# Performance work log

Hardware: AMD Instinct MI355X
Metric: run time of the kernel (lower is better)

## Reference

```python
import jax, jax.numpy as jnp
import numpy as np

MUL = 128          # multiplicity for every irrep
N = 100000         # number of nodes
INV_SQRT_FANIN = 1.0 / np.sqrt(MUL).astype(np.float32)


def setup_inputs() -> dict:
    key = jax.random.key(0)
    k = jax.random.split(key, 5)
    return {
        "x": jax.random.normal(k[0], (N, MUL + 3 * MUL), dtype=jnp.float32),   # [N, 512] = 128x0e + 128x1o
        "w1_s": jax.random.normal(k[1], (MUL, 2 * MUL), dtype=jnp.float32),    # 0e path of linear_1 (-> scalars+gates)
        "w1_v": jax.random.normal(k[2], (MUL, MUL), dtype=jnp.float32),        # 1o path of linear_1
        "w2_s": jax.random.normal(k[3], (MUL, MUL), dtype=jnp.float32),        # 0e path of linear_2
        "w2_v": jax.random.normal(k[4], (MUL, MUL), dtype=jnp.float32),        # 1o path of linear_2
    }


def reference(x, w1_s, w1_v, w2_s, w2_v):
    n = x.shape[0]
    x0 = x[:, :MUL]                              # [N, 128]  scalars (0e)
    x1 = x[:, MUL:].reshape(n, MUL, 3)           # [N, 128, 3] vectors (1o)

    # linear_1: 128x0e+128x1o -> 256x0e + 128x1o (scalars | gates | gated)
    s = (x0 @ w1_s) * INV_SQRT_FANIN             # [N, 256]
    v = jnp.einsum('nui,uv->nvi', x1, w1_v) * INV_SQRT_FANIN  # [N, 128, 3]

    # Gate: silu on scalars, silu(gates) broadcast-multiplies the vectors
    h0 = jax.nn.silu(s[:, :MUL])                 # [N, 128]
    g = jax.nn.silu(s[:, MUL:])                  # [N, 128]
    h1 = v * g[:, :, None]                       # [N, 128, 3]

    # linear_2: 128x0e+128x1o -> 128x0e+128x1o
    y0 = (h0 @ w2_s) * INV_SQRT_FANIN            # [N, 128]
    y1 = jnp.einsum('nui,uv->nvi', h1, w2_v) * INV_SQRT_FANIN  # [N, 128, 3]
    return jnp.concatenate([y0, y1.reshape(n, 3 * MUL)], axis=-1)  # [N, 512]
```

## Files before the change

kernel.cpp:

```cpp
#include <hip/hip_runtime.h>
#include <cstdint>

#define TPB  512
#define ROWS 32

typedef __attribute__((ext_vector_type(8))) short  short8;
typedef __attribute__((ext_vector_type(8))) __bf16 bf16x8;
typedef __attribute__((ext_vector_type(4))) float  f32x4;
typedef __attribute__((ext_vector_type(4))) short  short4v;

__device__ __forceinline__ short f2bf(float f) {
    union { float f; unsigned int u; } v; v.f = f;
    unsigned int u = v.u;
    u += 0x7fffu + ((u >> 16) & 1u);
    return (short)(u >> 16);
}
__device__ __forceinline__ float silu_f(float x) { return x / (1.0f + __expf(-x)); }

#define RSB 256
#define OFF_X0 0
#define OFF_X1 8192
#define OFF_H0 32768
#define SMEM_BYTES 40960

__device__ __forceinline__ int swz(int row, int b) { return row * RSB + (b ^ ((row & 7) << 4)); }

__device__ __forceinline__ short8 lds_bfrag(const char* sm, int off, int r0, int ks, int lane) {
    int row = r0 + (lane & 15);
    int bi  = ks * 64 + ((lane >> 4) << 4);
    return *(const short8*)(sm + off + swz(row, bi));
}

template<bool PACKED>
__device__ __forceinline__ short8 wfrag(const short8* pw, const float* W, int ldn,
                                        int gtile, int ltile, int ks, int lane) {
    if constexpr (PACKED) {
        return pw[(gtile * 4 + ks) * 64 + lane];
    } else {
        const float* p = W + (size_t)(ks * 32 + ((lane >> 4) << 3)) * ldn + ltile * 16 + (lane & 15);
        short8 r;
#pragma unroll
        for (int j = 0; j < 8; ++j) r[j] = f2bf(p[(size_t)j * ldn]);
        return r;
    }
}

__device__ __forceinline__ f32x4 mfma16(short8 a, short8 b, f32x4 c) {
    return __builtin_amdgcn_mfma_f32_16x16x32_bf16(
        __builtin_bit_cast(bf16x8, a), __builtin_bit_cast(bf16x8, b), c, 0, 0, 0);
}

__global__ void prep_pack(const float* __restrict__ w1s, const float* __restrict__ w1v,
                          const float* __restrict__ w2s, const float* __restrict__ w2v,
                          short8* __restrict__ pk) {
    int b = blockIdx.x;
    int t = threadIdx.x;
    int ks = t >> 6, lane = t & 63;
    const float* W; int ldn, lt;
    if (b < 16)      { W = w1s; ldn = 256; lt = b; }
    else if (b < 24) { W = w1v; ldn = 128; lt = b - 16; }
    else if (b < 32) { W = w2s; ldn = 128; lt = b - 24; }
    else             { W = w2v; ldn = 128; lt = b - 32; }
    const float* p = W + (size_t)(ks * 32 + ((lane >> 4) << 3)) * ldn + lt * 16 + (lane & 15);
    short8 r;
#pragma unroll
    for (int j = 0; j < 8; ++j) r[j] = f2bf(p[(size_t)j * ldn]);
    pk[(b * 4 + ks) * 64 + lane] = r;
}

template<bool PACKED>
__global__ __launch_bounds__(TPB, 8) void gnlr_fused_kernel(
    const float* __restrict__ x,
    const float* __restrict__ w1s, const float* __restrict__ w1v,
    const float* __restrict__ w2s, const float* __restrict__ w2v,
    const short8* __restrict__ pw,
    float* __restrict__ out, int n)
{
    __shared__ alignas(16) char sm[SMEM_BYTES];

    const int tid   = threadIdx.x;
    const int lane  = tid & 63;
    const int w     = tid >> 6;
    const int row0g = blockIdx.x * ROWS;
    const int c0    = w * 16;
    const float INV = 0.08838834764831845f;
    const f32x4 z = { 0.f, 0.f, 0.f, 0.f };

#pragma unroll
    for (int it = 0; it < 2; ++it) {
        int idx = tid + it * TPB;
        int row = idx >> 5;
        int c4  = (idx & 31) << 2;
        int rg  = row0g + row; if (rg >= n) rg = n - 1;
        float4 f = *(const float4*)(x + (size_t)rg * 512 + c4);
        short4v pkv;
        pkv.x = f2bf(f.x); pkv.y = f2bf(f.y); pkv.z = f2bf(f.z); pkv.w = f2bf(f.w);
        *(short4v*)(sm + OFF_X0 + swz(row, c4 * 2)) = pkv;
    }
#pragma unroll
    for (int it = 0; it < 2; ++it) {
        int idx = tid + it * TPB;
        int row = idx >> 5;
        int grp = idx & 31;
        int rg  = row0g + row; if (rg >= n) rg = n - 1;
        const float* p = x + (size_t)rg * 512 + 128 + grp * 12;
        float4 fa = *(const float4*)(p);
        float4 fb = *(const float4*)(p + 4);
        float4 fc = *(const float4*)(p + 8);
        float f[12] = { fa.x, fa.y, fa.z, fa.w, fb.x, fb.y, fb.z, fb.w, fc.x, fc.y, fc.z, fc.w };
#pragma unroll
        for (int i = 0; i < 3; ++i) {
            short4v pkv;
            pkv.x = f2bf(f[i]); pkv.y = f2bf(f[3 + i]); pkv.z = f2bf(f[6 + i]); pkv.w = f2bf(f[9 + i]);
            *(short4v*)(sm + OFF_X1 + i * 8192 + swz(row, grp * 8)) = pkv;
        }
    }
    __syncthreads();

    float g_reg[2][4];
    {
        short8 bs[4];
#pragma unroll
        for (int ks = 0; ks < 4; ++ks) bs[ks] = wfrag<PACKED>(pw, w1s, 256, w, w, ks, lane);
#pragma unroll
        for (int rt = 0; rt < 2; ++rt) {
            f32x4 acc = z;
#pragma unroll
            for (int ks = 0; ks < 4; ++ks)
                acc = mfma16(bs[ks], lds_bfrag(sm, OFF_X0, rt * 16, ks, lane), acc);
            short4v pkv;
#pragma unroll
            for (int j = 0; j < 4; ++j) pkv[j] = f2bf(silu_f(acc[j] * INV));
            int row = rt * 16 + (lane & 15);
            *(short4v*)(sm + OFF_H0 + swz(row, 2 * (c0 + ((lane >> 4) << 2)))) = pkv;
        }
#pragma unroll
        for (int ks = 0; ks < 4; ++ks) bs[ks] = wfrag<PACKED>(pw, w1s, 256, 8 + w, 8 + w, ks, lane);
#pragma unroll
        for (int rt = 0; rt < 2; ++rt) {
            f32x4 acc = z;
#pragma unroll
            for (int ks = 0; ks < 4; ++ks)
                acc = mfma16(bs[ks], lds_bfrag(sm, OFF_X0, rt * 16, ks, lane), acc);
#pragma unroll
            for (int j = 0; j < 4; ++j) g_reg[rt][j] = silu_f(acc[j] * INV);
        }
    }

    {
        short8 bv[4];
#pragma unroll
        for (int ks = 0; ks < 4; ++ks) bv[ks] = wfrag<PACKED>(pw, w1v, 128, 16 + w, w, ks, lane);
#pragma unroll
        for (int i = 0; i < 3; ++i) {
            __syncthreads();
#pragma unroll
            for (int rt = 0; rt < 2; ++rt) {
                f32x4 acc = z;
#pragma unroll
                for (int ks = 0; ks < 4; ++ks)
                    acc = mfma16(bv[ks], lds_bfrag(sm, OFF_X1 + i * 8192, rt * 16, ks, lane), acc);
                short4v pkv;
#pragma unroll
                for (int j = 0; j < 4; ++j) pkv[j] = f2bf(acc[j] * INV * g_reg[rt][j]);
                int row = rt * 16 + (lane & 15);
                *(short4v*)(sm + i * 8192 + swz(row, 2 * (c0 + ((lane >> 4) << 2)))) = pkv;
            }
        }
    }
    __syncthreads();

    {
        short8 b2[4];
#pragma unroll
        for (int ks = 0; ks < 4; ++ks) b2[ks] = wfrag<PACKED>(pw, w2s, 128, 24 + w, w, ks, lane);
#pragma unroll
        for (int rt = 0; rt < 2; ++rt) {
            f32x4 acc = z;
#pragma unroll
            for (int ks = 0; ks < 4; ++ks)
                acc = mfma16(b2[ks], lds_bfrag(sm, OFF_H0, rt * 16, ks, lane), acc);
            int rg = row0g + rt * 16 + (lane & 15);
            if (rg < n) {
                float4 o = { acc[0] * INV, acc[1] * INV, acc[2] * INV, acc[3] * INV };
                *(float4*)(out + (size_t)rg * 512 + c0 + ((lane >> 4) << 2)) = o;
            }
        }
#pragma unroll
        for (int ks = 0; ks < 4; ++ks) b2[ks] = wfrag<PACKED>(pw, w2v, 128, 32 + w, w, ks, lane);
#pragma unroll
        for (int rt = 0; rt < 2; ++rt) {
            f32x4 a3[3];
#pragma unroll
            for (int i = 0; i < 3; ++i) {
                a3[i] = z;
#pragma unroll
                for (int ks = 0; ks < 4; ++ks)
                    a3[i] = mfma16(b2[ks], lds_bfrag(sm, i * 8192, rt * 16, ks, lane), a3[i]);
            }
            int rg = row0g + rt * 16 + (lane & 15);
            if (rg < n) {
                float* base = out + (size_t)rg * 512 + 128 + 3 * (c0 + ((lane >> 4) << 2));
                float4 s0 = { a3[0][0] * INV, a3[1][0] * INV, a3[2][0] * INV, a3[0][1] * INV };
                float4 s1 = { a3[1][1] * INV, a3[2][1] * INV, a3[0][2] * INV, a3[1][2] * INV };
                float4 s2 = { a3[2][2] * INV, a3[0][3] * INV, a3[1][3] * INV, a3[2][3] * INV };
                *(float4*)(base + 0) = s0;
                *(float4*)(base + 4) = s1;
                *(float4*)(base + 8) = s2;
            }
        }
    }
}

extern "C" void kernel_launch(void* const* d_in, const int* in_sizes, int n_in,
                              void* d_out, int out_size, void* d_ws, size_t ws_size,
                              hipStream_t stream) {
    const float* x   = (const float*)d_in[0];
    const float* w1s = (const float*)d_in[1];
    const float* w1v = (const float*)d_in[2];
    const float* w2s = (const float*)d_in[3];
    const float* w2v = (const float*)d_in[4];
    float* out = (float*)d_out;
    const int n = in_sizes[0] / 512;
    const int grid = (n + ROWS - 1) / ROWS;
    const size_t need = (size_t)40 * 4 * 64 * sizeof(short8);
    if (ws_size >= need) {
        prep_pack<<<40, 256, 0, stream>>>(w1s, w1v, w2s, w2v, (short8*)d_ws);
        gnlr_fused_kernel<true><<<grid, TPB, 0, stream>>>(x, w1s, w1v, w2s, w2v,
                                                          (const short8*)d_ws, out, n);
    } else {
        gnlr_fused_kernel<false><<<grid, TPB, 0, stream>>>(x, w1s, w1v, w2s, w2v,
                                                           nullptr, out, n);
    }
}
```

Measured before the change: 107.5 us.

## Shrink block to 16 rows and 4 waves, each wave covering two column tiles

The block now handles 16 rows with 256 threads instead of 32 rows with 512, which halves LDS per block to 20 KB. Each wave now computes two column tiles over one 16-row tile, so the loops are reorganised from row tiles to column tiles. The aim is more resident blocks and finer scheduling granularity. In exchange, each weight fragment is reused over half as many rows, so weight fragment loads per output row double, and the w1v fragments are now reloaded inside each of the three vector-component passes.

```diff
diff --git a/kernel.cpp b/kernel.cpp
--- a/kernel.cpp
+++ b/kernel.cpp
@@ -1,8 +1,8 @@
 #include <hip/hip_runtime.h>
 #include <cstdint>
 
-#define TPB  512
-#define ROWS 32
+#define TPB  256
+#define ROWS 16
 
 typedef __attribute__((ext_vector_type(8))) short  short8;
 typedef __attribute__((ext_vector_type(8))) __bf16 bf16x8;
@@ -18,15 +18,14 @@
 __device__ __forceinline__ float silu_f(float x) { return x / (1.0f + __expf(-x)); }
 
 #define RSB 256
-#define OFF_X0 0
-#define OFF_X1 8192
-#define OFF_H0 32768
-#define SMEM_BYTES 40960
+#define OFF_X1 4096
+#define OFF_H0 16384
+#define SMEM_BYTES 20480
 
 __device__ __forceinline__ int swz(int row, int b) { return row * RSB + (b ^ ((row & 7) << 4)); }
 
-__device__ __forceinline__ short8 lds_bfrag(const char* sm, int off, int r0, int ks, int lane) {
-    int row = r0 + (lane & 15);
+__device__ __forceinline__ short8 lds_bfrag(const char* sm, int off, int ks, int lane) {
+    int row = lane & 15;
     int bi  = ks * 64 + ((lane >> 4) << 4);
     return *(const short8*)(sm + off + swz(row, bi));
 }
@@ -82,7 +81,6 @@
     const int lane  = tid & 63;
     const int w     = tid >> 6;
     const int row0g = blockIdx.x * ROWS;
-    const int c0    = w * 16;
     const float INV = 0.08838834764831845f;
     const f32x4 z = { 0.f, 0.f, 0.f, 0.f };
 
@@ -95,7 +93,7 @@
         float4 f = *(const float4*)(x + (size_t)rg * 512 + c4);
         short4v pkv;
         pkv.x = f2bf(f.x); pkv.y = f2bf(f.y); pkv.z = f2bf(f.z); pkv.w = f2bf(f.w);
-        *(short4v*)(sm + OFF_X0 + swz(row, c4 * 2)) = pkv;
+        *(short4v*)(sm + swz(row, c4 * 2)) = pkv;
     }
 #pragma unroll
     for (int it = 0; it < 2; ++it) {
@@ -112,93 +110,93 @@
         for (int i = 0; i < 3; ++i) {
             short4v pkv;
             pkv.x = f2bf(f[i]); pkv.y = f2bf(f[3 + i]); pkv.z = f2bf(f[6 + i]); pkv.w = f2bf(f[9 + i]);
-            *(short4v*)(sm + OFF_X1 + i * 8192 + swz(row, grp * 8)) = pkv;
+            *(short4v*)(sm + OFF_X1 + i * 4096 + swz(row, grp * 8)) = pkv;
         }
     }
     __syncthreads();
 
     float g_reg[2][4];
-    {
+#pragma unroll
+    for (int ut = 0; ut < 2; ++ut) {
+        int t0 = w + 4 * ut;
+        int c0 = t0 * 16;
         short8 bs[4];
 #pragma unroll
-        for (int ks = 0; ks < 4; ++ks) bs[ks] = wfrag<PACKED>(pw, w1s, 256, w, w, ks, lane);
-#pragma unroll
-        for (int rt = 0; rt < 2; ++rt) {
-            f32x4 acc = z;
-#pragma unroll
-            for (int ks = 0; ks < 4; ++ks)
-                acc = mfma16(bs[ks], lds_bfrag(sm, OFF_X0, rt * 16, ks, lane), acc);
+        for (int ks = 0; ks < 4; ++ks) bs[ks] = wfrag<PACKED>(pw, w1s, 256, t0, t0, ks, lane);
+        {
+            f32x4 acc = z;
+#pragma unroll
+            for (int ks = 0; ks < 4; ++ks)
+                acc = mfma16(bs[ks], lds_bfrag(sm, 0, ks, lane), acc);
             short4v pkv;
 #pragma unroll
             for (int j = 0; j < 4; ++j) pkv[j] = f2bf(silu_f(acc[j] * INV));
-            int row = rt * 16 + (lane & 15);
-            *(short4v*)(sm + OFF_H0 + swz(row, 2 * (c0 + ((lane >> 4) << 2)))) = pkv;
-        }
-#pragma unroll
-        for (int ks = 0; ks < 4; ++ks) bs[ks] = wfrag<PACKED>(pw, w1s, 256, 8 + w, 8 + w, ks, lane);
-#pragma unroll
-        for (int rt = 0; rt < 2; ++rt) {
-            f32x4 acc = z;
-#pragma unroll
-            for (int ks = 0; ks < 4; ++ks)
-                acc = mfma16(bs[ks], lds_bfrag(sm, OFF_X0, rt * 16, ks, lane), acc);
-#pragma unroll
-            for (int j = 0; j < 4; ++j) g_reg[rt][j] = silu_f(acc[j] * INV);
-        }
-    }
-
-    {
-        short8 bv[4];
-#pragma unroll
-        for (int ks = 0; ks < 4; ++ks) bv[ks] = wfrag<PACKED>(pw, w1v, 128, 16 + w, w, ks, lane);
-#pragma unroll
-        for (int i = 0; i < 3; ++i) {
-            __syncthreads();
-#pragma unroll
-            for (int rt = 0; rt < 2; ++rt) {
-                f32x4 acc = z;
-#pragma unroll
-                for (int ks = 0; ks < 4; ++ks)
-                    acc = mfma16(bv[ks], lds_bfrag(sm, OFF_X1 + i * 8192, rt * 16, ks, lane), acc);
-                short4v pkv;
-#pragma unroll
-                for (int j = 0; j < 4; ++j) pkv[j] = f2bf(acc[j] * INV * g_reg[rt][j]);
-                int row = rt * 16 + (lane & 15);
-                *(short4v*)(sm + i * 8192 + swz(row, 2 * (c0 + ((lane >> 4) << 2)))) = pkv;
-            }
+            *(short4v*)(sm + OFF_H0 + swz(lane & 15, 2 * (c0 + ((lane >> 4) << 2)))) = pkv;
+        }
+#pragma unroll
+        for (int ks = 0; ks < 4; ++ks) bs[ks] = wfrag<PACKED>(pw, w1s, 256, 8 + t0, 8 + t0, ks, lane);
+        {
+            f32x4 acc = z;
+#pragma unroll
+            for (int ks = 0; ks < 4; ++ks)
+                acc = mfma16(bs[ks], lds_bfrag(sm, 0, ks, lane), acc);
+#pragma unroll
+            for (int j = 0; j < 4; ++j) g_reg[ut][j] = silu_f(acc[j] * INV);
+        }
+    }
+
+#pragma unroll
+    for (int i = 0; i < 3; ++i) {
+        __syncthreads();
+#pragma unroll
+        for (int ut = 0; ut < 2; ++ut) {
+            int t0 = w + 4 * ut;
+            int c0 = t0 * 16;
+            short8 bv[4];
+#pragma unroll
+            for (int ks = 0; ks < 4; ++ks) bv[ks] = wfrag<PACKED>(pw, w1v, 128, 16 + t0, t0, ks, lane);
+            f32x4 acc = z;
+#pragma unroll
+            for (int ks = 0; ks < 4; ++ks)
+                acc = mfma16(bv[ks], lds_bfrag(sm, OFF_X1 + i * 4096, ks, lane), acc);
+            short4v pkv;
+#pragma unroll
+            for (int j = 0; j < 4; ++j) pkv[j] = f2bf(acc[j] * INV * g_reg[ut][j]);
+            *(short4v*)(sm + i * 4096 + swz(lane & 15, 2 * (c0 + ((lane >> 4) << 2)))) = pkv;
         }
     }
     __syncthreads();
 
-    {
+#pragma unroll
+    for (int ut = 0; ut < 2; ++ut) {
+        int t0 = w + 4 * ut;
+        int c0 = t0 * 16;
         short8 b2[4];
 #pragma unroll
-        for (int ks = 0; ks < 4; ++ks) b2[ks] = wfrag<PACKED>(pw, w2s, 128, 24 + w, w, ks, lane);
-#pragma unroll
-        for (int rt = 0; rt < 2; ++rt) {
-            f32x4 acc = z;
-#pragma unroll
-            for (int ks = 0; ks < 4; ++ks)
-                acc = mfma16(b2[ks], lds_bfrag(sm, OFF_H0, rt * 16, ks, lane), acc);
-            int rg = row0g + rt * 16 + (lane & 15);
+        for (int ks = 0; ks < 4; ++ks) b2[ks] = wfrag<PACKED>(pw, w2s, 128, 24 + t0, t0, ks, lane);
+        {
+            f32x4 acc = z;
+#pragma unroll
+            for (int ks = 0; ks < 4; ++ks)
+                acc = mfma16(b2[ks], lds_bfrag(sm, OFF_H0, ks, lane), acc);
+            int rg = row0g + (lane & 15);
             if (rg < n) {
                 float4 o = { acc[0] * INV, acc[1] * INV, acc[2] * INV, acc[3] * INV };
                 *(float4*)(out + (size_t)rg * 512 + c0 + ((lane >> 4) << 2)) = o;
             }
         }
 #pragma unroll
-        for (int ks = 0; ks < 4; ++ks) b2[ks] = wfrag<PACKED>(pw, w2v, 128, 32 + w, w, ks, lane);
-#pragma unroll
-        for (int rt = 0; rt < 2; ++rt) {
+        for (int ks = 0; ks < 4; ++ks) b2[ks] = wfrag<PACKED>(pw, w2v, 128, 32 + t0, t0, ks, lane);
+        {
             f32x4 a3[3];
 #pragma unroll
             for (int i = 0; i < 3; ++i) {
                 a3[i] = z;
 #pragma unroll
                 for (int ks = 0; ks < 4; ++ks)
-                    a3[i] = mfma16(b2[ks], lds_bfrag(sm, i * 8192, rt * 16, ks, lane), a3[i]);
+                    a3[i] = mfma16(b2[ks], lds_bfrag(sm, i * 4096, ks, lane), a3[i]);
             }
-            int rg = row0g + rt * 16 + (lane & 15);
+            int rg = row0g + (lane & 15);
             if (rg < n) {
                 float* base = out + (size_t)rg * 512 + 128 + 3 * (c0 + ((lane >> 4) << 2));
                 float4 s0 = { a3[0][0] * INV, a3[1][0] * INV, a3[2][0] * INV, a3[0][1] * INV };
```

Result: slower. 196.8 us (+83.0%).

## Make fused kernel persistent with atomic tile scheduling and double-buffered prefetch

Applied to the files above, without the earlier changes.

Turns the one-block-per-tile fused kernel into a persistent kernel with a fixed grid of 512 blocks. Blocks claim 32-row tiles through an atomic counter, which is reset by a memset before launch. Each block prefetches the next tile's x into registers while it computes the current tile, then writes it to a second LDS buffer. This is meant to hide global load latency and cut per-block launch and setup cost, but it raises LDS use to 72KB per block, lowers launch bounds occupancy to 4, and adds an atomic plus a barrier per tile. Tail handling is dropped (ntile = n/ROWS, no row bounds checks), so rows beyond a multiple of 32 would never be computed.

```diff
diff --git a/kernel.cpp b/kernel.cpp
--- a/kernel.cpp
+++ b/kernel.cpp
@@ -1,8 +1,9 @@
 #include <hip/hip_runtime.h>
 #include <cstdint>
 
-#define TPB  512
-#define ROWS 32
+#define TPB   512
+#define ROWS  32
+#define PGRID 512
 
 typedef __attribute__((ext_vector_type(8))) short  short8;
 typedef __attribute__((ext_vector_type(8))) __bf16 bf16x8;
@@ -18,17 +19,16 @@
 __device__ __forceinline__ float silu_f(float x) { return x / (1.0f + __expf(-x)); }
 
 #define RSB 256
-#define OFF_X0 0
-#define OFF_X1 8192
-#define OFF_H0 32768
-#define SMEM_BYTES 40960
+#define BUFSZ 32768
+#define OFF_H0 65536
+#define SMEM_BYTES 73728
 
 __device__ __forceinline__ int swz(int row, int b) { return row * RSB + (b ^ ((row & 7) << 4)); }
 
-__device__ __forceinline__ short8 lds_bfrag(const char* sm, int off, int r0, int ks, int lane) {
+__device__ __forceinline__ short8 lds_bfrag(const char* base, int off, int r0, int ks, int lane) {
     int row = r0 + (lane & 15);
     int bi  = ks * 64 + ((lane >> 4) << 4);
-    return *(const short8*)(sm + off + swz(row, bi));
+    return *(const short8*)(base + off + swz(row, bi));
 }
 
 template<bool PACKED>
@@ -53,8 +53,7 @@
 __global__ void prep_pack(const float* __restrict__ w1s, const float* __restrict__ w1v,
                           const float* __restrict__ w2s, const float* __restrict__ w2v,
                           short8* __restrict__ pk) {
-    int b = blockIdx.x;
-    int t = threadIdx.x;
+    int b = blockIdx.x, t = threadIdx.x;
     int ks = t >> 6, lane = t & 63;
     const float* W; int ldn, lt;
     if (b < 16)      { W = w1s; ldn = 256; lt = b; }
@@ -69,137 +68,178 @@
 }
 
 template<bool PACKED>
-__global__ __launch_bounds__(TPB, 8) void gnlr_fused_kernel(
+__global__ __launch_bounds__(TPB, 4) void gnlr_fused_kernel(
     const float* __restrict__ x,
     const float* __restrict__ w1s, const float* __restrict__ w1v,
     const float* __restrict__ w2s, const float* __restrict__ w2v,
-    const short8* __restrict__ pw,
-    float* __restrict__ out, int n)
+    const short8* __restrict__ pw, unsigned int* __restrict__ ctr,
+    float* __restrict__ out, int ntile)
 {
-    __shared__ alignas(16) char sm[SMEM_BYTES];
-
-    const int tid   = threadIdx.x;
-    const int lane  = tid & 63;
-    const int w     = tid >> 6;
-    const int row0g = blockIdx.x * ROWS;
-    const int c0    = w * 16;
+    extern __shared__ char sm[];
+    __shared__ int s_tile;
+
+    const int tid  = threadIdx.x;
+    const int lane = tid & 63;
+    const int w    = tid >> 6;
+    const int c0   = w * 16;
     const float INV = 0.08838834764831845f;
     const f32x4 z = { 0.f, 0.f, 0.f, 0.f };
 
-#pragma unroll
-    for (int it = 0; it < 2; ++it) {
-        int idx = tid + it * TPB;
-        int row = idx >> 5;
-        int c4  = (idx & 31) << 2;
-        int rg  = row0g + row; if (rg >= n) rg = n - 1;
-        float4 f = *(const float4*)(x + (size_t)rg * 512 + c4);
-        short4v pkv;
-        pkv.x = f2bf(f.x); pkv.y = f2bf(f.y); pkv.z = f2bf(f.z); pkv.w = f2bf(f.w);
-        *(short4v*)(sm + OFF_X0 + swz(row, c4 * 2)) = pkv;
-    }
-#pragma unroll
-    for (int it = 0; it < 2; ++it) {
-        int idx = tid + it * TPB;
-        int row = idx >> 5;
-        int grp = idx & 31;
-        int rg  = row0g + row; if (rg >= n) rg = n - 1;
-        const float* p = x + (size_t)rg * 512 + 128 + grp * 12;
-        float4 fa = *(const float4*)(p);
-        float4 fb = *(const float4*)(p + 4);
-        float4 fc = *(const float4*)(p + 8);
-        float f[12] = { fa.x, fa.y, fa.z, fa.w, fb.x, fb.y, fb.z, fb.w, fc.x, fc.y, fc.z, fc.w };
-#pragma unroll
-        for (int i = 0; i < 3; ++i) {
-            short4v pkv;
-            pkv.x = f2bf(f[i]); pkv.y = f2bf(f[3 + i]); pkv.z = f2bf(f[6 + i]); pkv.w = f2bf(f[9 + i]);
-            *(short4v*)(sm + OFF_X1 + i * 8192 + swz(row, grp * 8)) = pkv;
-        }
-    }
-    __syncthreads();
-
-    float g_reg[2][4];
-    {
-        short8 bs[4];
-#pragma unroll
-        for (int ks = 0; ks < 4; ++ks) bs[ks] = wfrag<PACKED>(pw, w1s, 256, w, w, ks, lane);
-#pragma unroll
-        for (int rt = 0; rt < 2; ++rt) {
-            f32x4 acc = z;
-#pragma unroll
-            for (int ks = 0; ks < 4; ++ks)
-                acc = mfma16(bs[ks], lds_bfrag(sm, OFF_X0, rt * 16, ks, lane), acc);
-            short4v pkv;
-#pragma unroll
-            for (int j = 0; j < 4; ++j) pkv[j] = f2bf(silu_f(acc[j] * INV));
-            int row = rt * 16 + (lane & 15);
-            *(short4v*)(sm + OFF_H0 + swz(row, 2 * (c0 + ((lane >> 4) << 2)))) = pkv;
-        }
-#pragma unroll
-        for (int ks = 0; ks < 4; ++ks) bs[ks] = wfrag<PACKED>(pw, w1s, 256, 8 + w, 8 + w, ks, lane);
-#pragma unroll
-        for (int rt = 0; rt < 2; ++rt) {
-            f32x4 acc = z;
-#pragma unroll
-            for (int ks = 0; ks < 4; ++ks)
-                acc = mfma16(bs[ks], lds_bfrag(sm, OFF_X0, rt * 16, ks, lane), acc);
-#pragma unroll
-            for (int j = 0; j < 4; ++j) g_reg[rt][j] = silu_f(acc[j] * INV);
-        }
-    }
-
-    {
-        short8 bv[4];
-#pragma unroll
-        for (int ks = 0; ks < 4; ++ks) bv[ks] = wfrag<PACKED>(pw, w1v, 128, 16 + w, w, ks, lane);
-#pragma unroll
-        for (int i = 0; i < 3; ++i) {
+    float4 st[8];
+    int nextStatic = blockIdx.x;
+
+    auto grab = [&]() -> int {
+        int r;
+        if constexpr (PACKED) {
+            if (tid == 0) s_tile = (int)atomicAdd(ctr, 1u);
             __syncthreads();
+            r = s_tile;
+        } else {
+            r = nextStatic; nextStatic += PGRID;
+            __syncthreads();
+        }
+        return r;
+    };
+
+    auto issue = [&](int tile) {
+        const float* xb = x + (size_t)tile * ROWS * 512;
+#pragma unroll
+        for (int it = 0; it < 2; ++it) {
+            int idx = tid + it * TPB;
+            int row = idx >> 5, c4 = (idx & 31) << 2;
+            st[it] = *(const float4*)(xb + row * 512 + c4);
+        }
+#pragma unroll
+        for (int it = 0; it < 2; ++it) {
+            int idx = tid + it * TPB;
+            int row = idx >> 5, grp = idx & 31;
+            const float* p = xb + row * 512 + 128 + grp * 12;
+            st[2 + it * 3 + 0] = *(const float4*)(p);
+            st[2 + it * 3 + 1] = *(const float4*)(p + 4);
+            st[2 + it * 3 + 2] = *(const float4*)(p + 8);
+        }
+    };
+
+    auto writeLDS = [&](int buf) {
+        char* b = sm + buf * BUFSZ;
+#pragma unroll
+        for (int it = 0; it < 2; ++it) {
+            int idx = tid + it * TPB;
+            int row = idx >> 5, c4 = (idx & 31) << 2;
+            float4 f = st[it];
+            short4v pk;
+            pk.x = f2bf(f.x); pk.y = f2bf(f.y); pk.z = f2bf(f.z); pk.w = f2bf(f.w);
+            *(short4v*)(b + swz(row, c4 * 2)) = pk;
+        }
+#pragma unroll
+        for (int it = 0; it < 2; ++it) {
+            int idx = tid + it * TPB;
+            int row = idx >> 5, grp = idx & 31;
+            float4 fa = st[2 + it * 3 + 0], fb = st[2 + it * 3 + 1], fc = st[2 + it * 3 + 2];
+            float fv[12] = { fa.x, fa.y, fa.z, fa.w, fb.x, fb.y, fb.z, fb.w, fc.x, fc.y, fc.z, fc.w };
+#pragma unroll
+            for (int i = 0; i < 3; ++i) {
+                short4v pk;
+                pk.x = f2bf(fv[i]); pk.y = f2bf(fv[3 + i]); pk.z = f2bf(fv[6 + i]); pk.w = f2bf(fv[9 + i]);
+                *(short4v*)(b + 8192 + i * 8192 + swz(row, grp * 8)) = pk;
+            }
+        }
+    };
+
+    int tcur = grab();
+    if (tcur >= ntile) return;
+    issue(tcur);
+    writeLDS(0);
+    int cur = 0;
+
+    while (true) {
+        int tnext = grab();
+        bool hasN = tnext < ntile;
+        if (hasN) issue(tnext);
+
+        char* B = sm + cur * BUFSZ;
+        const int row0g = tcur * ROWS;
+
+        float g_reg[2][4];
+        {
+            short8 bs[4];
+#pragma unroll
+            for (int ks = 0; ks < 4; ++ks) bs[ks] = wfrag<PACKED>(pw, w1s, 256, w, w, ks, lane);
 #pragma unroll
             for (int rt = 0; rt < 2; ++rt) {
                 f32x4 acc = z;
 #pragma unroll
                 for (int ks = 0; ks < 4; ++ks)
-                    acc = mfma16(bv[ks], lds_bfrag(sm, OFF_X1 + i * 8192, rt * 16, ks, lane), acc);
+                    acc = mfma16(bs[ks], lds_bfrag(B, 0, rt * 16, ks, lane), acc);
                 short4v pkv;
 #pragma unroll
-                for (int j = 0; j < 4; ++j) pkv[j] = f2bf(acc[j] * INV * g_reg[rt][j]);
+                for (int j = 0; j < 4; ++j) pkv[j] = f2bf(silu_f(acc[j] * INV));
                 int row = rt * 16 + (lane & 15);
-                *(short4v*)(sm + i * 8192 + swz(row, 2 * (c0 + ((lane >> 4) << 2)))) = pkv;
-            }
-        }
-    }
-    __syncthreads();
-
-    {
-        short8 b2[4];
-#pragma unroll
-        for (int ks = 0; ks < 4; ++ks) b2[ks] = wfrag<PACKED>(pw, w2s, 128, 24 + w, w, ks, lane);
-#pragma unroll
-        for (int rt = 0; rt < 2; ++rt) {
-            f32x4 acc = z;
-#pragma unroll
-            for (int ks = 0; ks < 4; ++ks)
-                acc = mfma16(b2[ks], lds_bfrag(sm, OFF_H0, rt * 16, ks, lane), acc);
-            int rg = row0g + rt * 16 + (lane & 15);
-            if (rg < n) {
+                *(short4v*)(sm + OFF_H0 + swz(row, 2 * (c0 + ((lane >> 4) << 2)))) = pkv;
+            }
+#pragma unroll
+            for (int ks = 0; ks < 4; ++ks) bs[ks] = wfrag<PACKED>(pw, w1s, 256, 8 + w, 8 + w, ks, lane);
+#pragma unroll
+            for (int rt = 0; rt < 2; ++rt) {
+                f32x4 acc = z;
+#pragma unroll
+                for (int ks = 0; ks < 4; ++ks)
+                    acc = mfma16(bs[ks], lds_bfrag(B, 0, rt * 16, ks, lane), acc);
+#pragma unroll
+                for (int j = 0; j < 4; ++j) g_reg[rt][j] = silu_f(acc[j] * INV);
+            }
+        }
+
+        {
+            short8 bv[4];
+#pragma unroll
+            for (int ks = 0; ks < 4; ++ks) bv[ks] = wfrag<PACKED>(pw, w1v, 128, 16 + w, w, ks, lane);
+#pragma unroll
+            for (int i = 0; i < 3; ++i) {
+                __syncthreads();
+#pragma unroll
+                for (int rt = 0; rt < 2; ++rt) {
+                    f32x4 acc = z;
+#pragma unroll
+                    for (int ks = 0; ks < 4; ++ks)
+                        acc = mfma16(bv[ks], lds_bfrag(B, 8192 + i * 8192, rt * 16, ks, lane), acc);
+                    short4v pkv;
+#pragma unroll
+                    for (int j = 0; j < 4; ++j) pkv[j] = f2bf(acc[j] * INV * g_reg[rt][j]);
+                    int row = rt * 16 + (lane & 15);
+                    *(short4v*)(B + i * 8192 + swz(row, 2 * (c0 + ((lane >> 4) << 2)))) = pkv;
+                }
+            }
+        }
+        __syncthreads();
+
+        {
+            short8 b2[4];
+#pragma unroll
+            for (int ks = 0; ks < 4; ++ks) b2[ks] = wfrag<PACKED>(pw, w2s, 128, 24 + w, w, ks, lane);
+#pragma unroll
+            for (int rt = 0; rt < 2; ++rt) {
+                f32x4 acc = z;
+#pragma unroll
+                for (int ks = 0; ks < 4; ++ks)
+                    acc = mfma16(b2[ks], lds_bfrag(sm, OFF_H0, rt * 16, ks, lane), acc);
+                int rg = row0g + rt * 16 + (lane & 15);
                 float4 o = { acc[0] * INV, acc[1] * INV, acc[2] * INV, acc[3] * INV };
                 *(float4*)(out + (size_t)rg * 512 + c0 + ((lane >> 4) << 2)) = o;
             }
-        }
-#pragma unroll
-        for (int ks = 0; ks < 4; ++ks) b2[ks] = wfrag<PACKED>(pw, w2v, 128, 32 + w, w, ks, lane);
-#pragma unroll
-        for (int rt = 0; rt < 2; ++rt) {
-            f32x4 a3[3];
-#pragma unroll
-            for (int i = 0; i < 3; ++i) {
-                a3[i] = z;
-#pragma unroll
-                for (int ks = 0; ks < 4; ++ks)
-                    a3[i] = mfma16(b2[ks], lds_bfrag(sm, i * 8192, rt * 16, ks, lane), a3[i]);
-            }
-            int rg = row0g + rt * 16 + (lane & 15);
-            if (rg < n) {
+#pragma unroll
+            for (int ks = 0; ks < 4; ++ks) b2[ks] = wfrag<PACKED>(pw, w2v, 128, 32 + w, w, ks, lane);
+#pragma unroll
+            for (int rt = 0; rt < 2; ++rt) {
+                f32x4 a3[3];
+#pragma unroll
+                for (int i = 0; i < 3; ++i) {
+                    a3[i] = z;
+#pragma unroll
+                    for (int ks = 0; ks < 4; ++ks)
+                        a3[i] = mfma16(b2[ks], lds_bfrag(B, i * 8192, rt * 16, ks, lane), a3[i]);
+                }
+                int rg = row0g + rt * 16 + (lane & 15);
                 float* base = out + (size_t)rg * 512 + 128 + 3 * (c0 + ((lane >> 4) << 2));
                 float4 s0 = { a3[0][0] * INV, a3[1][0] * INV, a3[2][0] * INV, a3[0][1] * INV };
                 float4 s1 = { a3[1][1] * INV, a3[2][1] * INV, a3[0][2] * INV, a3[1][2] * INV };
@@ -209,6 +249,11 @@
                 *(float4*)(base + 8) = s2;
             }
         }
+
+        if (!hasN) break;
+        writeLDS(cur ^ 1);
+        cur ^= 1;
+        tcur = tnext;
     }
 }
 
@@ -222,14 +267,16 @@
     const float* w2v = (const float*)d_in[4];
     float* out = (float*)d_out;
     const int n = in_sizes[0] / 512;
-    const int grid = (n + ROWS - 1) / ROWS;
-    const size_t need = (size_t)40 * 4 * 64 * sizeof(short8);
-    if (ws_size >= need) {
+    const int ntile = n / ROWS;
+    const size_t needW = (size_t)40 * 4 * 64 * sizeof(short8);
+    if (ws_size >= needW + 4) {
+        unsigned int* ctr = (unsigned int*)((char*)d_ws + needW);
+        hipMemsetAsync(ctr, 0, 4, stream);
         prep_pack<<<40, 256, 0, stream>>>(w1s, w1v, w2s, w2v, (short8*)d_ws);
-        gnlr_fused_kernel<true><<<grid, TPB, 0, stream>>>(x, w1s, w1v, w2s, w2v,
-                                                          (const short8*)d_ws, out, n);
+        gnlr_fused_kernel<true><<<PGRID, TPB, SMEM_BYTES, stream>>>(
+            x, w1s, w1v, w2s, w2v, (const short8*)d_ws, ctr, out, ntile);
     } else {
-        gnlr_fused_kernel<false><<<grid, TPB, 0, stream>>>(x, w1s, w1v, w2s, w2v,
-                                                           nullptr, out, n);
+        gnlr_fused_kernel<false><<<PGRID, TPB, SMEM_BYTES, stream>>>(
+            x, w1s, w1v, w2s, w2v, nullptr, nullptr, out, ntile);
     }
 }
```

Result: slower. 301.5 us (+180.5%).

## Process two row tiles per block with register-prefetched loads and nontemporal stores

Applied to the files above, without the earlier changes.

Each block now handles two 32-row tiles. The global loads for the second tile are issued into registers while the first tile computes, hiding load latency behind the MFMA work. Output stores become nontemporal, and launch bounds drop to 4 blocks per CU to make room for the extra registers. The tail clamping is removed and the grid uses n/32, so when n is not a multiple of 32 the leftover rows are never computed. This is fine for N=100000, but it adds register pressure and may lower occupancy.

```diff
diff --git a/kernel.cpp b/kernel.cpp
--- a/kernel.cpp
+++ b/kernel.cpp
@@ -17,18 +17,20 @@
 }
 __device__ __forceinline__ float silu_f(float x) { return x / (1.0f + __expf(-x)); }
 
+__device__ __forceinline__ void nt_st4(float* p, f32x4 v) {
+    __builtin_nontemporal_store(v, (f32x4*)p);
+}
+
 #define RSB 256
-#define OFF_X0 0
-#define OFF_X1 8192
 #define OFF_H0 32768
 #define SMEM_BYTES 40960
 
 __device__ __forceinline__ int swz(int row, int b) { return row * RSB + (b ^ ((row & 7) << 4)); }
 
-__device__ __forceinline__ short8 lds_bfrag(const char* sm, int off, int r0, int ks, int lane) {
+__device__ __forceinline__ short8 lds_bfrag(const char* base, int off, int r0, int ks, int lane) {
     int row = r0 + (lane & 15);
     int bi  = ks * 64 + ((lane >> 4) << 4);
-    return *(const short8*)(sm + off + swz(row, bi));
+    return *(const short8*)(base + off + swz(row, bi));
 }
 
 template<bool PACKED>
@@ -53,8 +55,7 @@
 __global__ void prep_pack(const float* __restrict__ w1s, const float* __restrict__ w1v,
                           const float* __restrict__ w2s, const float* __restrict__ w2v,
                           short8* __restrict__ pk) {
-    int b = blockIdx.x;
-    int t = threadIdx.x;
+    int b = blockIdx.x, t = threadIdx.x;
     int ks = t >> 6, lane = t & 63;
     const float* W; int ldn, lt;
     if (b < 16)      { W = w1s; ldn = 256; lt = b; }
@@ -69,7 +70,7 @@
 }
 
 template<bool PACKED>
-__global__ __launch_bounds__(TPB, 8) void gnlr_fused_kernel(
+__global__ __launch_bounds__(TPB, 4) void gnlr_fused_kernel(
     const float* __restrict__ x,
     const float* __restrict__ w1s, const float* __restrict__ w1v,
     const float* __restrict__ w2s, const float* __restrict__ w2v,
@@ -81,134 +82,169 @@
     const int tid   = threadIdx.x;
     const int lane  = tid & 63;
     const int w     = tid >> 6;
-    const int row0g = blockIdx.x * ROWS;
     const int c0    = w * 16;
     const float INV = 0.08838834764831845f;
     const f32x4 z = { 0.f, 0.f, 0.f, 0.f };
 
-#pragma unroll
-    for (int it = 0; it < 2; ++it) {
-        int idx = tid + it * TPB;
-        int row = idx >> 5;
-        int c4  = (idx & 31) << 2;
-        int rg  = row0g + row; if (rg >= n) rg = n - 1;
-        float4 f = *(const float4*)(x + (size_t)rg * 512 + c4);
-        short4v pkv;
-        pkv.x = f2bf(f.x); pkv.y = f2bf(f.y); pkv.z = f2bf(f.z); pkv.w = f2bf(f.w);
-        *(short4v*)(sm + OFF_X0 + swz(row, c4 * 2)) = pkv;
-    }
-#pragma unroll
-    for (int it = 0; it < 2; ++it) {
-        int idx = tid + it * TPB;
-        int row = idx >> 5;
-        int grp = idx & 31;
-        int rg  = row0g + row; if (rg >= n) rg = n - 1;
-        const float* p = x + (size_t)rg * 512 + 128 + grp * 12;
-        float4 fa = *(const float4*)(p);
-        float4 fb = *(const float4*)(p + 4);
-        float4 fc = *(const float4*)(p + 8);
-        float f[12] = { fa.x, fa.y, fa.z, fa.w, fb.x, fb.y, fb.z, fb.w, fc.x, fc.y, fc.z, fc.w };
-#pragma unroll
-        for (int i = 0; i < 3; ++i) {
-            short4v pkv;
-            pkv.x = f2bf(f[i]); pkv.y = f2bf(f[3 + i]); pkv.z = f2bf(f[6 + i]); pkv.w = f2bf(f[9 + i]);
-            *(short4v*)(sm + OFF_X1 + i * 8192 + swz(row, grp * 8)) = pkv;
-        }
-    }
+    const int ntile = n >> 5;
+    const int t0 = blockIdx.x * 2;
+    const int t1 = t0 + 1;
+    const bool has1 = (t1 < ntile);
+
+    float4 st[8];
+
+    auto issue = [&](int tile) {
+        const float* xb = x + (size_t)tile * ROWS * 512;
+#pragma unroll
+        for (int it = 0; it < 2; ++it) {
+            int idx = tid + it * TPB;
+            int row = idx >> 5, c4 = (idx & 31) << 2;
+            st[it] = *(const float4*)(xb + row * 512 + c4);
+        }
+#pragma unroll
+        for (int it = 0; it < 2; ++it) {
+            int idx = tid + it * TPB;
+            int row = idx >> 5, grp = idx & 31;
+            const float* p = xb + row * 512 + 128 + grp * 12;
+            st[2 + it * 3 + 0] = *(const float4*)(p);
+            st[2 + it * 3 + 1] = *(const float4*)(p + 4);
+            st[2 + it * 3 + 2] = *(const float4*)(p + 8);
+        }
+    };
+
+    auto writeLDS = [&]() {
+#pragma unroll
+        for (int it = 0; it < 2; ++it) {
+            int idx = tid + it * TPB;
+            int row = idx >> 5, c4 = (idx & 31) << 2;
+            float4 f = st[it];
+            short4v pk;
+            pk.x = f2bf(f.x); pk.y = f2bf(f.y); pk.z = f2bf(f.z); pk.w = f2bf(f.w);
+            *(short4v*)(sm + swz(row, c4 * 2)) = pk;
+        }
+#pragma unroll
+        for (int it = 0; it < 2; ++it) {
+            int idx = tid + it * TPB;
+            int row = idx >> 5, grp = idx & 31;
+            float4 fa = st[2 + it * 3 + 0], fb = st[2 + it * 3 + 1], fc = st[2 + it * 3 + 2];
+            float fv[12] = { fa.x, fa.y, fa.z, fa.w, fb.x, fb.y, fb.z, fb.w, fc.x, fc.y, fc.z, fc.w };
+#pragma unroll
+            for (int i = 0; i < 3; ++i) {
+                short4v pk;
+                pk.x = f2bf(fv[i]); pk.y = f2bf(fv[3 + i]); pk.z = f2bf(fv[6 + i]); pk.w = f2bf(fv[9 + i]);
+                *(short4v*)(sm + 8192 + i * 8192 + swz(row, grp * 8)) = pk;
+            }
+        }
+    };
+
+    auto computeTile = [&](int tile) {
+        const int row0g = tile * ROWS;
+
+        float g_reg[2][4];
+        {
+            short8 bs[4];
+#pragma unroll
+            for (int ks = 0; ks < 4; ++ks) bs[ks] = wfrag<PACKED>(pw, w1s, 256, w, w, ks, lane);
+#pragma unroll
+            for (int rt = 0; rt < 2; ++rt) {
+                f32x4 acc = z;
+#pragma unroll
+                for (int ks = 0; ks < 4; ++ks)
+                    acc = mfma16(bs[ks], lds_bfrag(sm, 0, rt * 16, ks, lane), acc);
+                short4v pkv;
+#pragma unroll
+                for (int j = 0; j < 4; ++j) pkv[j] = f2bf(silu_f(acc[j] * INV));
+                int row = rt * 16 + (lane & 15);
+                *(short4v*)(sm + OFF_H0 + swz(row, 2 * (c0 + ((lane >> 4) << 2)))) = pkv;
+            }
+#pragma unroll
+            for (int ks = 0; ks < 4; ++ks) bs[ks] = wfrag<PACKED>(pw, w1s, 256, 8 + w, 8 + w, ks, lane);
+#pragma unroll
+            for (int rt = 0; rt < 2; ++rt) {
+                f32x4 acc = z;
+#pragma unroll
+                for (int ks = 0; ks < 4; ++ks)
+                    acc = mfma16(bs[ks], lds_bfrag(sm, 0, rt * 16, ks, lane), acc);
+#pragma unroll
+                for (int j = 0; j < 4; ++j) g_reg[rt][j] = silu_f(acc[j] * INV);
+            }
+        }
+
+        {
+            short8 bv[4];
+#pragma unroll
+            for (int ks = 0; ks < 4; ++ks) bv[ks] = wfrag<PACKED>(pw, w1v, 128, 16 + w, w, ks, lane);
+#pragma unroll
+            for (int i = 0; i < 3; ++i) {
+                __syncthreads();
+#pragma unroll
+                for (int rt = 0; rt < 2; ++rt) {
+                    f32x4 acc = z;
+#pragma unroll
+                    for (int ks = 0; ks < 4; ++ks)
+                        acc = mfma16(bv[ks], lds_bfrag(sm, 8192 + i * 8192, rt * 16, ks, lane), acc);
+                    short4v pkv;
+#pragma unroll
+                    for (int j = 0; j < 4; ++j) pkv[j] = f2bf(acc[j] * INV * g_reg[rt][j]);
+                    int row = rt * 16 + (lane & 15);
+                    *(short4v*)(sm + i * 8192 + swz(row, 2 * (c0 + ((lane >> 4) << 2)))) = pkv;
+                }
+            }
+        }
+        __syncthreads();
+
+        {
+            short8 b2[4];
+#pragma unroll
+            for (int ks = 0; ks < 4; ++ks) b2[ks] = wfrag<PACKED>(pw, w2s, 128, 24 + w, w, ks, lane);
+#pragma unroll
+            for (int rt = 0; rt < 2; ++rt) {
+                f32x4 acc = z;
+#pragma unroll
+                for (int ks = 0; ks < 4; ++ks)
+                    acc = mfma16(b2[ks], lds_bfrag(sm, OFF_H0, rt * 16, ks, lane), acc);
+                int rg = row0g + rt * 16 + (lane & 15);
+                if (rg < n) {
+                    f32x4 o = { acc[0] * INV, acc[1] * INV, acc[2] * INV, acc[3] * INV };
+                    nt_st4(out + (size_t)rg * 512 + c0 + ((lane >> 4) << 2), o);
+                }
+            }
+#pragma unroll
+            for (int ks = 0; ks < 4; ++ks) b2[ks] = wfrag<PACKED>(pw, w2v, 128, 32 + w, w, ks, lane);
+#pragma unroll
+            for (int rt = 0; rt < 2; ++rt) {
+                f32x4 a3[3];
+#pragma unroll
+                for (int i = 0; i < 3; ++i) {
+                    a3[i] = z;
+#pragma unroll
+                    for (int ks = 0; ks < 4; ++ks)
+                        a3[i] = mfma16(b2[ks], lds_bfrag(sm, i * 8192, rt * 16, ks, lane), a3[i]);
+                }
+                int rg = row0g + rt * 16 + (lane & 15);
+                if (rg < n) {
+                    float* base = out + (size_t)rg * 512 + 128 + 3 * (c0 + ((lane >> 4) << 2));
+                    f32x4 s0 = { a3[0][0] * INV, a3[1][0] * INV, a3[2][0] * INV, a3[0][1] * INV };
+                    f32x4 s1 = { a3[1][1] * INV, a3[2][1] * INV, a3[0][2] * INV, a3[1][2] * INV };
+                    f32x4 s2 = { a3[2][2] * INV, a3[0][3] * INV, a3[1][3] * INV, a3[2][3] * INV };
+                    nt_st4(base + 0, s0);
+                    nt_st4(base + 4, s1);
+                    nt_st4(base + 8, s2);
+                }
+            }
+        }
+    };
+
+    issue(t0);
+    writeLDS();
     __syncthreads();
-
-    float g_reg[2][4];
-    {
-        short8 bs[4];
-#pragma unroll
-        for (int ks = 0; ks < 4; ++ks) bs[ks] = wfrag<PACKED>(pw, w1s, 256, w, w, ks, lane);
-#pragma unroll
-        for (int rt = 0; rt < 2; ++rt) {
-            f32x4 acc = z;
-#pragma unroll
-            for (int ks = 0; ks < 4; ++ks)
-                acc = mfma16(bs[ks], lds_bfrag(sm, OFF_X0, rt * 16, ks, lane), acc);
-            short4v pkv;
-#pragma unroll
-            for (int j = 0; j < 4; ++j) pkv[j] = f2bf(silu_f(acc[j] * INV));
-            int row = rt * 16 + (lane & 15);
-            *(short4v*)(sm + OFF_H0 + swz(row, 2 * (c0 + ((lane >> 4) << 2)))) = pkv;
-        }
-#pragma unroll
-        for (int ks = 0; ks < 4; ++ks) bs[ks] = wfrag<PACKED>(pw, w1s, 256, 8 + w, 8 + w, ks, lane);
-#pragma unroll
-        for (int rt = 0; rt < 2; ++rt) {
-            f32x4 acc = z;
-#pragma unroll
-            for (int ks = 0; ks < 4; ++ks)
-                acc = mfma16(bs[ks], lds_bfrag(sm, OFF_X0, rt * 16, ks, lane), acc);
-#pragma unroll
-            for (int j = 0; j < 4; ++j) g_reg[rt][j] = silu_f(acc[j] * INV);
-        }
-    }
-
-    {
-        short8 bv[4];
-#pragma unroll
-        for (int ks = 0; ks < 4; ++ks) bv[ks] = wfrag<PACKED>(pw, w1v, 128, 16 + w, w, ks, lane);
-#pragma unroll
-        for (int i = 0; i < 3; ++i) {
-            __syncthreads();
-#pragma unroll
-            for (int rt = 0; rt < 2; ++rt) {
-                f32x4 acc = z;
-#pragma unroll
-                for (int ks = 0; ks < 4; ++ks)
-                    acc = mfma16(bv[ks], lds_bfrag(sm, OFF_X1 + i * 8192, rt * 16, ks, lane), acc);
-                short4v pkv;
-#pragma unroll
-                for (int j = 0; j < 4; ++j) pkv[j] = f2bf(acc[j] * INV * g_reg[rt][j]);
-                int row = rt * 16 + (lane & 15);
-                *(short4v*)(sm + i * 8192 + swz(row, 2 * (c0 + ((lane >> 4) << 2)))) = pkv;
-            }
-        }
-    }
-    __syncthreads();
-
-    {
-        short8 b2[4];
-#pragma unroll
-        for (int ks = 0; ks < 4; ++ks) b2[ks] = wfrag<PACKED>(pw, w2s, 128, 24 + w, w, ks, lane);
-#pragma unroll
-        for (int rt = 0; rt < 2; ++rt) {
-            f32x4 acc = z;
-#pragma unroll
-            for (int ks = 0; ks < 4; ++ks)
-                acc = mfma16(b2[ks], lds_bfrag(sm, OFF_H0, rt * 16, ks, lane), acc);
-            int rg = row0g + rt * 16 + (lane & 15);
-            if (rg < n) {
-                float4 o = { acc[0] * INV, acc[1] * INV, acc[2] * INV, acc[3] * INV };
-                *(float4*)(out + (size_t)rg * 512 + c0 + ((lane >> 4) << 2)) = o;
-            }
-        }
-#pragma unroll
-        for (int ks = 0; ks < 4; ++ks) b2[ks] = wfrag<PACKED>(pw, w2v, 128, 32 + w, w, ks, lane);
-#pragma unroll
-        for (int rt = 0; rt < 2; ++rt) {
-            f32x4 a3[3];
-#pragma unroll
-            for (int i = 0; i < 3; ++i) {
-                a3[i] = z;
-#pragma unroll
-                for (int ks = 0; ks < 4; ++ks)
-                    a3[i] = mfma16(b2[ks], lds_bfrag(sm, i * 8192, rt * 16, ks, lane), a3[i]);
-            }
-            int rg = row0g + rt * 16 + (lane & 15);
-            if (rg < n) {
-                float* base = out + (size_t)rg * 512 + 128 + 3 * (c0 + ((lane >> 4) << 2));
-                float4 s0 = { a3[0][0] * INV, a3[1][0] * INV, a3[2][0] * INV, a3[0][1] * INV };
-                float4 s1 = { a3[1][1] * INV, a3[2][1] * INV, a3[0][2] * INV, a3[1][2] * INV };
-                float4 s2 = { a3[2][2] * INV, a3[0][3] * INV, a3[1][3] * INV, a3[2][3] * INV };
-                *(float4*)(base + 0) = s0;
-                *(float4*)(base + 4) = s1;
-                *(float4*)(base + 8) = s2;
-            }
-        }
+    if (has1) issue(t1);
+    computeTile(t0);
+    if (has1) {
+        __syncthreads();
+        writeLDS();
+        __syncthreads();
+        computeTile(t1);
     }
 }
 
@@ -222,7 +258,8 @@
     const float* w2v = (const float*)d_in[4];
     float* out = (float*)d_out;
     const int n = in_sizes[0] / 512;
-    const int grid = (n + ROWS - 1) / ROWS;
+    const int ntile = n / ROWS;
+    const int grid = (ntile + 1) / 2;
     const size_t need = (size_t)40 * 4 * 64 * sizeof(short8);
     if (ws_size >= need) {
         prep_pack<<<40, 256, 0, stream>>>(w1s, w1v, w2s, w2v, (short8*)d_ws);
```

After: 125.4 us. +16.7%, slower.
